# Performance work log

Measured on AMD Instinct MI355X. Metric: run time of the kernel, lower is better.

The kernel has to match this reference:

```python
import jax, jax.numpy as jnp
import numpy as np

B, T, M, D, H, DK, DV = 2, 1024, 1024, 1024, 16, 64, 64
R = 2 * T + M  # number of relative positions required by rel_shift path


def setup_inputs() -> dict:
    key = jax.random.key(0)
    ks = jax.random.split(key, 11)
    s = 0.02
    return {
        "inputs": jax.random.normal(ks[0], (B, T, D), jnp.float32),
        "attention_mask": jnp.ones((B, T, M + T), jnp.float32),
        "positional_encodings": jax.random.normal(ks[1], (R, D), jnp.float32),
        "memory": jax.random.normal(ks[2], (B, M, D), jnp.float32),
        "Wq": jax.random.normal(ks[3], (D, H * DK), jnp.float32) * s,
        "Wk": jax.random.normal(ks[4], (D, H * DK), jnp.float32) * s,
        "Wv": jax.random.normal(ks[5], (D, H * DV), jnp.float32) * s,
        "Wr": jax.random.normal(ks[6], (D, H * DK), jnp.float32) * s,
        "r_w_bias": jax.random.normal(ks[7], (H, DK), jnp.float32) * s,
        "r_r_bias": jax.random.normal(ks[8], (H, DK), jnp.float32) * s,
        "W_out": jax.random.normal(ks[9], (H * DV, D), jnp.float32) * s,
    }


def _rel_shift(m, attention_length):
    # m: [T_q, T_q + L] -> [T_q, L], TXL relative shift via reshape/slice
    tq, total = m.shape
    x = m.reshape(total, tq)[1:].reshape(tq, total - 1)
    return x[:, :attention_length]


def reference(inputs, attention_mask, positional_encodings, memory,
              Wq, Wk, Wv, Wr, r_w_bias, r_r_bias, W_out):
    b, t, d = inputs.shape
    values = jnp.concatenate([memory, inputs], axis=1)  # [B, L, D]
    L = values.shape[1]
    q = (inputs @ Wq).reshape(b, t, H, DK)
    k = (values @ Wk).reshape(b, L, H, DK)
    v = (values @ Wv).reshape(b, L, H, DV)
    rk = (positional_encodings @ Wr).reshape(-1, H, DK)  # [R, H, DK]
    # content + relative logits (TXL)
    content = jnp.einsum('bthd,bThd->bhtT', q + r_w_bias, k)        # [B,H,T,L]
    rel = jnp.einsum('bthd,rhd->bhtr', q + r_r_bias, rk)            # [B,H,T,R]
    rel = jax.vmap(jax.vmap(lambda m: _rel_shift(m, L)))(rel)       # [B,H,T,L]
    logits = (content + rel) * (DK ** -0.5)
    masked = logits - (1.0 - attention_mask[:, None, :, :]) * 1e30
    w = jax.nn.softmax(masked, axis=-1)
    attn = jnp.einsum('bhtT,bThd->bthd', w, v)                      # [B,T,H,DV]
    return attn.reshape(b, t, H * DV) @ W_out
```

## Files before the change

### kernel.cpp

```cpp
#include <hip/hip_runtime.h>
#include <hip/hip_fp16.h>
#include <stdint.h>

#define Bz 2
#define Tq 1024
#define Mm 1024
#define Hh 16
#define Ll 2048
#define Rr 3072

typedef __attribute__((ext_vector_type(8))) short bf16x8;
typedef __attribute__((ext_vector_type(4))) float f32x4;

typedef __attribute__((address_space(3))) uint8_t lds_u8_t;
typedef __attribute__((address_space(1))) uint8_t glb_u8_t;

__device__ __forceinline__ void gl2lds16(const void* g, void* l) {
  __builtin_amdgcn_global_load_lds((const glb_u8_t*)g, (lds_u8_t*)l, 16, 0, 0);
}

__device__ __forceinline__ unsigned short f2bf(float f) {
  unsigned int u = __builtin_bit_cast(unsigned int, f);
  u = u + 0x7fffu + ((u >> 16) & 1u);
  return (unsigned short)(u >> 16);
}
__device__ __forceinline__ float b2f(unsigned short s) {
  unsigned int u = ((unsigned int)s) << 16;
  return __builtin_bit_cast(float, u);
}

__global__ __launch_bounds__(256) void k_prep2(
    const float* __restrict__ x, const float* __restrict__ mem,
    const float* __restrict__ pos, const float* __restrict__ mask,
    const float* __restrict__ w0, const float* __restrict__ w1,
    const float* __restrict__ w2, const float* __restrict__ w3,
    const float* __restrict__ w4,
    unsigned short* __restrict__ vin, unsigned short* __restrict__ pb,
    unsigned short* __restrict__ mb,
    unsigned short* __restrict__ t0, unsigned short* __restrict__ t1,
    unsigned short* __restrict__ t2, unsigned short* __restrict__ t3,
    unsigned short* __restrict__ t4) {
  __shared__ float tile[64][65];
  int bid = blockIdx.x;
  if (bid < 4096) {
    int idx = bid * 256 + threadIdx.x;
    int e = idx << 2;
    int row = e >> 10, col = e & 1023;
    int b = row >> 11, l = row & 2047;
    const float* s = (l < Mm) ? (mem + (((size_t)b * Mm + l) << 10) + col)
                              : (x + (((size_t)b * Tq + (l - Mm)) << 10) + col);
    float4 v = *(const float4*)s;
    ushort4 o;
    o.x = f2bf(v.x); o.y = f2bf(v.y); o.z = f2bf(v.z); o.w = f2bf(v.w);
    *(ushort4*)(vin + e) = o;
  } else if (bid < 7168) {
    int idx = (bid - 4096) * 256 + threadIdx.x;
    int e = idx << 2;
    float4 v = *(const float4*)(pos + e);
    ushort4 t;
    t.x = f2bf(v.x); t.y = f2bf(v.y); t.z = f2bf(v.z); t.w = f2bf(v.w);
    *(ushort4*)(pb + e) = t;
  } else if (bid < 11264) {
    int idx = (bid - 7168) * 256 + threadIdx.x;
    int e = idx << 2;
    const float BIGM = 1.442695e30f;
    float4 v = *(const float4*)(mask + e);
    ushort4 t;
    t.x = f2bf((1.0f - v.x) * BIGM); t.y = f2bf((1.0f - v.y) * BIGM);
    t.z = f2bf((1.0f - v.z) * BIGM); t.w = f2bf((1.0f - v.w) * BIGM);
    *(ushort4*)(mb + e) = t;
  } else {
    int r3 = bid - 11264;
    int mz = r3 >> 8, rem = r3 & 255;
    const float* W;
    unsigned short* WT;
    switch (mz) {
      case 0: W = w0; WT = t0; break;
      case 1: W = w1; WT = t1; break;
      case 2: W = w2; WT = t2; break;
      case 3: W = w3; WT = t3; break;
      default: W = w4; WT = t4; break;
    }
    int k0 = (rem >> 4) * 64, n0 = (rem & 15) * 64;
    int tid = threadIdx.x;
    int rr = tid >> 4, c4 = (tid & 15) * 4;
#pragma unroll
    for (int it = 0; it < 4; ++it) {
      int r = rr + it * 16;
      float4 v = *(const float4*)(W + (size_t)(k0 + r) * 1024 + n0 + c4);
      tile[r][c4] = v.x; tile[r][c4 + 1] = v.y;
      tile[r][c4 + 2] = v.z; tile[r][c4 + 3] = v.w;
    }
    __syncthreads();
#pragma unroll
    for (int it = 0; it < 4; ++it) {
      int n = rr + it * 16;
      ushort4 o;
      o.x = f2bf(tile[c4 + 0][n]); o.y = f2bf(tile[c4 + 1][n]);
      o.z = f2bf(tile[c4 + 2][n]); o.w = f2bf(tile[c4 + 3][n]);
      *(ushort4*)(WT + (size_t)(n0 + n) * 1024 + k0 + c4) = o;
    }
  }
}

template <int RMAP>
__device__ __forceinline__ void gemm_pipe(const unsigned short* __restrict__ A,
                                          const unsigned short* __restrict__ Bt,
                                          int m0, int n0, unsigned short* As,
                                          unsigned short* Bs, f32x4 acc[4][4]) {
  const int tid = threadIdx.x;
  const int w = tid >> 6, lane = tid & 63;
  const int quad = lane >> 4, li = lane & 15;
  const int wr = w >> 1, wc = w & 1;
  f32x4 z = {0.f, 0.f, 0.f, 0.f};
#pragma unroll
  for (int mi = 0; mi < 4; ++mi)
#pragma unroll
    for (int ni = 0; ni < 4; ++ni) acc[mi][ni] = z;

  const int rs = lane >> 2;
  const int cs = lane & 3;

#pragma unroll
  for (int s = 0; s < 2; ++s) {
    int i = w * 2 + s;
    int r = i * 16 + rs;
    int c = cs ^ ((r >> 1) & 3);
    int ar = m0 + r;
    if (RMAP) ar = ar + 1024 + (ar & 1024);
    gl2lds16(A + (size_t)ar * 1024 + c * 8, (char*)As + i * 1024);
    gl2lds16(Bt + (size_t)(n0 + r) * 1024 + c * 8, (char*)Bs + i * 1024);
  }

  for (int k0 = 0; k0 < 1024; k0 += 32) {
    const int bo = ((k0 >> 5) & 1) * 8192;
    const int no = bo ^ 8192;
    __builtin_amdgcn_s_waitcnt(0x0F70);
    __syncthreads();
    if (k0 + 32 < 1024) {
#pragma unroll
      for (int s = 0; s < 2; ++s) {
        int i = w * 2 + s;
        int r = i * 16 + rs;
        int c = cs ^ ((r >> 1) & 3);
        int ar = m0 + r;
        if (RMAP) ar = ar + 1024 + (ar & 1024);
        gl2lds16(A + (size_t)ar * 1024 + k0 + 32 + c * 8,
                 (char*)As + no + i * 1024);
        gl2lds16(Bt + (size_t)(n0 + r) * 1024 + k0 + 32 + c * 8,
                 (char*)Bs + no + i * 1024);
      }
    }
    bf16x8 af[4], bfr[4];
#pragma unroll
    for (int mi = 0; mi < 4; ++mi) {
      int r = wr * 64 + mi * 16 + li;
      int ch = quad ^ ((r >> 1) & 3);
      af[mi] = *(const bf16x8*)((const char*)As + bo + r * 64 + ch * 16);
    }
#pragma unroll
    for (int ni = 0; ni < 4; ++ni) {
      int r = wc * 64 + ni * 16 + li;
      int ch = quad ^ ((r >> 1) & 3);
      bfr[ni] = *(const bf16x8*)((const char*)Bs + bo + r * 64 + ch * 16);
    }
#pragma unroll
    for (int mi = 0; mi < 4; ++mi)
#pragma unroll
      for (int ni = 0; ni < 4; ++ni)
        acc[mi][ni] = __builtin_amdgcn_mfma_f32_16x16x32_bf16(
            af[mi], bfr[ni], acc[mi][ni], 0, 0, 0);
  }
}

__global__ __launch_bounds__(256) void k_proj(
    const unsigned short* __restrict__ Vin, const unsigned short* __restrict__ Pb,
    const unsigned short* __restrict__ WqT, const unsigned short* __restrict__ WkT,
    const unsigned short* __restrict__ WvT, const unsigned short* __restrict__ WrT,
    unsigned short* __restrict__ qb, unsigned short* __restrict__ kb,
    unsigned short* __restrict__ vtb, unsigned short* __restrict__ rkb) {
  __shared__ unsigned short As[2 * 128 * 32];
  __shared__ unsigned short Bs[2 * 128 * 32];
  const int t = blockIdx.x;
  const int tid = threadIdx.x, w = tid >> 6, lane = tid & 63;
  const int quad = lane >> 4, li = lane & 15, wr = w >> 1, wc = w & 1;
  f32x4 acc[4][4];

  if (t < 256) {
    int m0 = (t >> 3) * 128, n0 = (t & 7) * 128;
    gemm_pipe<0>(Vin, WkT, m0, n0, As, Bs, acc);
#pragma unroll
    for (int mi = 0; mi < 4; ++mi)
#pragma unroll
      for (int ni = 0; ni < 4; ++ni)
#pragma unroll
        for (int reg = 0; reg < 4; ++reg) {
          int rrow = m0 + wr * 64 + mi * 16 + quad * 4 + reg;
          int cc = n0 + wc * 64 + ni * 16 + li;
          kb[(size_t)rrow * 1024 + cc] = f2bf(acc[mi][ni][reg]);
        }
  } else if (t < 512) {
    int tt = t - 256;
    int m0 = (tt >> 3) * 128, n0 = (tt & 7) * 128;
    gemm_pipe<0>(Vin, WvT, m0, n0, As, Bs, acc);
#pragma unroll
    for (int mi = 0; mi < 4; ++mi)
#pragma unroll
      for (int ni = 0; ni < 4; ++ni) {
        int r0 = m0 + wr * 64 + mi * 16 + quad * 4;
        int b = r0 >> 11, l0 = r0 & 2047;
        int cc = n0 + wc * 64 + ni * 16 + li;
        ushort4 o;
        o.x = f2bf(acc[mi][ni][0]); o.y = f2bf(acc[mi][ni][1]);
        o.z = f2bf(acc[mi][ni][2]); o.w = f2bf(acc[mi][ni][3]);
        *(ushort4*)(vtb + ((size_t)(b * 1024 + cc)) * Ll + l0) = o;
      }
  } else if (t < 640) {
    int tt = t - 512;
    int m0 = (tt >> 3) * 128, n0 = (tt & 7) * 128;
    gemm_pipe<1>(Vin, WqT, m0, n0, As, Bs, acc);
#pragma unroll
    for (int mi = 0; mi < 4; ++mi)
#pragma unroll
      for (int ni = 0; ni < 4; ++ni)
#pragma unroll
        for (int reg = 0; reg < 4; ++reg) {
          int rrow = m0 + wr * 64 + mi * 16 + quad * 4 + reg;
          int cc = n0 + wc * 64 + ni * 16 + li;
          qb[(size_t)rrow * 1024 + cc] = f2bf(acc[mi][ni][reg]);
        }
  } else {
    int tt = t - 640;
    int m0 = (tt >> 3) * 128, n0 = (tt & 7) * 128;
    gemm_pipe<0>(Pb, WrT, m0, n0, As, Bs, acc);
#pragma unroll
    for (int mi = 0; mi < 4; ++mi)
#pragma unroll
      for (int ni = 0; ni < 4; ++ni)
#pragma unroll
        for (int reg = 0; reg < 4; ++reg) {
          int rrow = m0 + wr * 64 + mi * 16 + quad * 4 + reg;
          int cc = n0 + wc * 64 + ni * 16 + li;
          rkb[(size_t)rrow * 1024 + cc] = f2bf(acc[mi][ni][reg]);
        }
  }
}

__global__ __launch_bounds__(256) void k_gemm_out64(
    const unsigned short* __restrict__ attnb, const unsigned short* __restrict__ WoT,
    float* __restrict__ out) {
  __shared__ unsigned short As[2 * 64 * 32];
  __shared__ unsigned short Bs[2 * 128 * 32];
  int m0 = blockIdx.x * 64, n0 = blockIdx.y * 128;
  const int tid = threadIdx.x, w = tid >> 6, lane = tid & 63;
  const int quad = lane >> 4, li = lane & 15, wr = w >> 1, wc = w & 1;
  f32x4 z = {0.f, 0.f, 0.f, 0.f};
  f32x4 acc[2][4];
#pragma unroll
  for (int mi = 0; mi < 2; ++mi)
#pragma unroll
    for (int ni = 0; ni < 4; ++ni) acc[mi][ni] = z;
  const int rs = lane >> 2, cs = lane & 3;

  {
    int r = w * 16 + rs;
    int c = cs ^ ((r >> 1) & 3);
    gl2lds16(attnb + (size_t)(m0 + r) * 1024 + c * 8, (char*)As + w * 1024);
  }
#pragma unroll
  for (int s = 0; s < 2; ++s) {
    int i = w * 2 + s;
    int r = i * 16 + rs;
    int c = cs ^ ((r >> 1) & 3);
    gl2lds16(WoT + (size_t)(n0 + r) * 1024 + c * 8, (char*)Bs + i * 1024);
  }

  for (int k0 = 0; k0 < 1024; k0 += 32) {
    const int boa = ((k0 >> 5) & 1) * 4096;
    const int bob = ((k0 >> 5) & 1) * 8192;
    __builtin_amdgcn_s_waitcnt(0x0F70);
    __syncthreads();
    if (k0 + 32 < 1024) {
      {
        int r = w * 16 + rs;
        int c = cs ^ ((r >> 1) & 3);
        gl2lds16(attnb + (size_t)(m0 + r) * 1024 + k0 + 32 + c * 8,
                 (char*)As + (boa ^ 4096) + w * 1024);
      }
#pragma unroll
      for (int s = 0; s < 2; ++s) {
        int i = w * 2 + s;
        int r = i * 16 + rs;
        int c = cs ^ ((r >> 1) & 3);
        gl2lds16(WoT + (size_t)(n0 + r) * 1024 + k0 + 32 + c * 8,
                 (char*)Bs + (bob ^ 8192) + i * 1024);
      }
    }
    bf16x8 af[2], bfr[4];
#pragma unroll
    for (int mi = 0; mi < 2; ++mi) {
      int r = wr * 32 + mi * 16 + li;
      int ch = quad ^ ((r >> 1) & 3);
      af[mi] = *(const bf16x8*)((const char*)As + boa + r * 64 + ch * 16);
    }
#pragma unroll
    for (int ni = 0; ni < 4; ++ni) {
      int r = wc * 64 + ni * 16 + li;
      int ch = quad ^ ((r >> 1) & 3);
      bfr[ni] = *(const bf16x8*)((const char*)Bs + bob + r * 64 + ch * 16);
    }
#pragma unroll
    for (int mi = 0; mi < 2; ++mi)
#pragma unroll
      for (int ni = 0; ni < 4; ++ni)
        acc[mi][ni] = __builtin_amdgcn_mfma_f32_16x16x32_bf16(
            af[mi], bfr[ni], acc[mi][ni], 0, 0, 0);
  }
#pragma unroll
  for (int mi = 0; mi < 2; ++mi)
#pragma unroll
    for (int ni = 0; ni < 4; ++ni)
#pragma unroll
      for (int reg = 0; reg < 4; ++reg) {
        int rrow = m0 + wr * 32 + mi * 16 + quad * 4 + reg;
        int cc = n0 + wc * 64 + ni * 16 + li;
        out[(size_t)rrow * 1024 + cc] = acc[mi][ni][reg];
      }
}

__global__ __launch_bounds__(256, 2) void k_attn(
    const unsigned short* __restrict__ qb, const float* __restrict__ rwb,
    const float* __restrict__ rrb,
    const unsigned short* __restrict__ kb, const unsigned short* __restrict__ vt,
    const unsigned short* __restrict__ rkb, const unsigned short* __restrict__ mb,
    unsigned short* __restrict__ attnb) {
  __shared__ unsigned short Ks[2][64 * 64];
  __shared__ unsigned short Vs[2][64 * 64];
  __shared__ unsigned short Rs[256 * 64];
  __shared__ unsigned short Sb[4][16 * 72];

  const int tid = threadIdx.x;
  const int w = tid >> 6, lane = tid & 63;
  const int quad = lane >> 4, li = lane & 15;
  const int flat = blockIdx.x + 16 * blockIdx.y + 256 * blockIdx.z;
  const int qt = (flat >> 3) & 15;
  const int g = 4 * (flat & 7) + (flat >> 7);
  const int h = g & 15, b = g >> 4;
  const int t0blk = qt * 64;
  const int t0w = t0blk + w * 16;
  const int rboff = 48 - 16 * w;
  const int rbase0 = Tq - t0blk - 63;

  bf16x8 aqw[2], aqr[2];
  {
    const unsigned short* p1 = qb + ((size_t)((b * Tq + t0w + li) * Hh + h)) * 64;
#pragma unroll
    for (int ks = 0; ks < 2; ++ks) {
      bf16x8 qf = *(const bf16x8*)(p1 + ks * 32 + quad * 8);
      const float* wp = rwb + h * 64 + ks * 32 + quad * 8;
      const float* rp = rrb + h * 64 + ks * 32 + quad * 8;
      float4 w0 = *(const float4*)wp, w1 = *(const float4*)(wp + 4);
      float4 r0 = *(const float4*)rp, r1 = *(const float4*)(rp + 4);
      float wv[8] = {w0.x, w0.y, w0.z, w0.w, w1.x, w1.y, w1.z, w1.w};
      float rv[8] = {r0.x, r0.y, r0.z, r0.w, r1.x, r1.y, r1.z, r1.w};
#pragma unroll
      for (int i2 = 0; i2 < 8; ++i2) {
        float qv = b2f((unsigned short)qf[i2]);
        aqw[ks][i2] = (short)f2bf(qv + wv[i2]);
        aqr[ks][i2] = (short)f2bf(qv + rv[i2]);
      }
    }
  }

  f32x4 z = {0.f, 0.f, 0.f, 0.f};
  f32x4 o[4];
  o[0] = z; o[1] = z; o[2] = z; o[3] = z;
  f32x4 ol = z;

  const int srow = lane >> 3;
  const int scs = lane & 7;
  const float SC = 0.125f * 1.4426950408889634f;
  const short oneb = 0x3F80;
  const bf16x8 onesf = {oneb, oneb, oneb, oneb, oneb, oneb, oneb, oneb};

  unsigned short* pw = &Sb[w][0];
  const unsigned short* mrowA = mb + ((size_t)(b * Tq + t0w + li)) * Ll;
  int srcl[4];
#pragma unroll
  for (int reg = 0; reg < 4; ++reg) {
    int row = quad * 4 + reg;
    srcl[reg] = (lane & 48) + ((li + row + 1) & 15);
  }

  auto finish = [&](const unsigned short* VsP, bf16x8 mvF0, bf16x8 mvF1) {
    bf16x8 apv[2];
#pragma unroll
    for (int ks = 0; ks < 2; ++ks) {
      const int cofs = ks * 32 + quad * 8;
      ushort4 s0 = *(const ushort4*)(pw + li * 72 + cofs);
      ushort4 s1 = *(const ushort4*)(pw + li * 72 + cofs + 4);
      bf16x8 mv = ks ? mvF1 : mvF0;
      unsigned short su[8] = {s0.x, s0.y, s0.z, s0.w, s1.x, s1.y, s1.z, s1.w};
#pragma unroll
      for (int i2 = 0; i2 < 8; ++i2) {
        float sf = __half2float(__builtin_bit_cast(__half, su[i2]));
        float mvf = b2f((unsigned short)mv[i2]);
        float p = exp2f(sf * SC - mvf);
        apv[ks][i2] = (short)f2bf(p);
      }
    }
    __builtin_amdgcn_s_setprio(1);
#pragma unroll
    for (int ks = 0; ks < 2; ++ks)
      ol = __builtin_amdgcn_mfma_f32_16x16x32_bf16(apv[ks], onesf, ol, 0, 0, 0);
#pragma unroll
    for (int ks = 0; ks < 2; ++ks)
#pragma unroll
      for (int nt = 0; nt < 4; ++nt) {
        int dv = nt * 16 + li;
        int ch = (ks * 4 + quad) ^ (dv & 7);
        bf16x8 vf = *(const bf16x8*)((const char*)VsP + dv * 128 + ch * 16);
        o[nt] = __builtin_amdgcn_mfma_f32_16x16x32_bf16(apv[ks], vf, o[nt], 0, 0, 0);
      }
    __builtin_amdgcn_s_setprio(0);
  };

#pragma unroll
  for (int s = 0; s < 4; ++s) {
    int i = w * 4 + s;
    int r = i * 8 + srow;
    int gr = rbase0 + r;
    if (gr > Rr - 1) gr = Rr - 1;
    int c = scs ^ (r & 7);
    gl2lds16(rkb + ((size_t)gr * Hh + h) * 64 + c * 8, (char*)Rs + i * 1024);
  }
#pragma unroll
  for (int s = 0; s < 2; ++s) {
    int i = w * 2 + s;
    int r = i * 8 + srow;
    int c = scs ^ (r & 7);
    gl2lds16(kb + ((size_t)((b * Ll + r) * Hh + h)) * 64 + c * 8,
             (char*)Ks[0] + i * 1024);
  }
  bf16x8 nmv0 = {0, 0, 0, 0, 0, 0, 0, 0};
  bf16x8 nmv1 = {0, 0, 0, 0, 0, 0, 0, 0};

  for (int jt = 0; jt < 32; ++jt) {
    const int j0 = jt * 64;
    __builtin_amdgcn_s_waitcnt(0x0F70);
    __syncthreads();
    bf16x8 mvF0 = nmv0, mvF1 = nmv1;
    if (jt < 31) {
      const int j0n = j0 + 64;
#pragma unroll
      for (int s = 0; s < 2; ++s) {
        int i = w * 2 + s;
        int r = i * 8 + srow;
        int c = scs ^ (r & 7);
        gl2lds16(kb + ((size_t)((b * Ll + j0n + r) * Hh + h)) * 64 + c * 8,
                 (char*)Ks[(jt + 1) & 1] + i * 1024);
      }
#pragma unroll
      for (int s = 0; s < 2; ++s) {
        int i2 = w * 2 + s;
        int rr = i2 * 8 + srow;
        int ofs = j0 + 128 + rr;
        int gr = rbase0 + ofs;
        if (gr > Rr - 1) gr = Rr - 1;
        int ring = ofs & 255;
        int c = scs ^ (rr & 7);
        gl2lds16(rkb + ((size_t)gr * Hh + h) * 64 + c * 8, (char*)Rs + ring * 128);
      }
    }
#pragma unroll
    for (int s = 0; s < 2; ++s) {
      int i = w * 2 + s;
      int r = i * 8 + srow;
      int c = scs ^ (r & 7);
      gl2lds16(vt + ((size_t)((b * Hh + h) * 64 + r)) * Ll + j0 + c * 8,
               (char*)Vs[jt & 1] + i * 1024);
    }
    nmv0 = *(const bf16x8*)(mrowA + j0 + quad * 8);
    nmv1 = *(const bf16x8*)(mrowA + j0 + 32 + quad * 8);
    asm volatile("" ::: "memory");
    const unsigned short* KsC = Ks[jt & 1];
    f32x4 sc[4];
    sc[0] = z; sc[1] = z; sc[2] = z; sc[3] = z;
    __builtin_amdgcn_s_setprio(1);
#pragma unroll
    for (int ks = 0; ks < 2; ++ks)
#pragma unroll
      for (int nt = 0; nt < 4; ++nt) {
        int j = nt * 16 + li;
        int ch = (ks * 4 + quad) ^ (j & 7);
        bf16x8 kf = *(const bf16x8*)((const char*)KsC + j * 128 + ch * 16);
        sc[nt] = __builtin_amdgcn_mfma_f32_16x16x32_bf16(aqw[ks], kf, sc[nt], 0, 0, 0);
      }
    f32x4 bd[5];
    bd[0] = z; bd[1] = z; bd[2] = z; bd[3] = z; bd[4] = z;
#pragma unroll
    for (int ks = 0; ks < 2; ++ks)
#pragma unroll
      for (int nt = 0; nt < 5; ++nt) {
        int pr = (rboff + nt * 16 + li + j0) & 255;
        int ch = (ks * 4 + quad) ^ (pr & 7);
        bf16x8 rf = *(const bf16x8*)((const char*)Rs + pr * 128 + ch * 16);
        bd[nt] = __builtin_amdgcn_mfma_f32_16x16x32_bf16(aqr[ks], rf, bd[nt], 0, 0, 0);
      }
    __builtin_amdgcn_s_setprio(0);
    if (jt > 0) finish(Vs[(jt - 1) & 1], mvF0, mvF1);
    float rot[4][4];
#pragma unroll
    for (int nt = 0; nt < 4; ++nt)
#pragma unroll
      for (int reg = 0; reg < 4; ++reg)
        rot[nt][reg] = __shfl(sc[nt][reg], srcl[reg], 64);
#pragma unroll
    for (int nt = 0; nt < 5; ++nt)
#pragma unroll
      for (int reg = 0; reg < 4; ++reg) {
        int row = quad * 4 + reg;
        int jj = nt * 16 + li + row - 15;
        int ntlo = (nt == 0) ? 3 : (nt - 1);
        int nthi = (nt > 3) ? 0 : nt;
        float val = ((li + row) >= 15) ? rot[nthi][reg] : rot[ntlo][reg];
        float s = val + bd[nt][reg];
        if ((unsigned)jj < 64u)
          pw[row * 72 + jj] = __builtin_bit_cast(unsigned short, __float2half(s));
      }
  }
  __builtin_amdgcn_s_waitcnt(0x0F70);
  __syncthreads();
  finish(Vs[1], nmv0, nmv1);

  float inv[4];
#pragma unroll
  for (int reg = 0; reg < 4; ++reg) inv[reg] = 1.0f / ol[reg];
#pragma unroll
  for (int nt = 0; nt < 4; ++nt)
#pragma unroll
    for (int reg = 0; reg < 4; ++reg) {
      int trow = t0w + quad * 4 + reg;
      attnb[((size_t)(b * Tq + trow)) * 1024 + h * 64 + nt * 16 + li] =
          f2bf(o[nt][reg] * inv[reg]);
    }
}

extern "C" void kernel_launch(void* const* d_in, const int* in_sizes, int n_in,
                              void* d_out, int out_size, void* d_ws, size_t ws_size,
                              hipStream_t stream) {
  const float* x = (const float*)d_in[0];
  const float* mask = (const float*)d_in[1];
  const float* pos = (const float*)d_in[2];
  const float* mem = (const float*)d_in[3];
  const float* Wq = (const float*)d_in[4];
  const float* Wk = (const float*)d_in[5];
  const float* Wv = (const float*)d_in[6];
  const float* Wr = (const float*)d_in[7];
  const float* rwb = (const float*)d_in[8];
  const float* rrb = (const float*)d_in[9];
  const float* Wo = (const float*)d_in[10];
  float* out = (float*)d_out;

  uint8_t* ws = (uint8_t*)d_ws;
  const size_t MB = 1024 * 1024;
  unsigned short* Vinb = (unsigned short*)(ws + 0);
  unsigned short* WqT = (unsigned short*)(ws + 8 * MB);
  unsigned short* WkT = (unsigned short*)(ws + 10 * MB);
  unsigned short* WvT = (unsigned short*)(ws + 12 * MB);
  unsigned short* WrT = (unsigned short*)(ws + 14 * MB);
  unsigned short* WoT = (unsigned short*)(ws + 16 * MB);
  unsigned short* Pb = (unsigned short*)(ws + 18 * MB);
  unsigned short* qb = (unsigned short*)(ws + 24 * MB);
  unsigned short* kb = (unsigned short*)(ws + 32 * MB);
  unsigned short* vtb = (unsigned short*)(ws + 40 * MB);
  unsigned short* rkb = (unsigned short*)(ws + 48 * MB);
  unsigned short* mbb = (unsigned short*)(ws + 54 * MB);
  unsigned short* attnb = (unsigned short*)(ws + 19 * MB);

  hipLaunchKernelGGL(k_prep2, dim3(12544), dim3(256), 0, stream,
                     x, mem, pos, mask, Wq, Wk, Wv, Wr, Wo,
                     Vinb, Pb, mbb, WqT, WkT, WvT, WrT, WoT);
  hipLaunchKernelGGL(k_proj, dim3(832), dim3(256), 0, stream,
                     Vinb, Pb, WqT, WkT, WvT, WrT, qb, kb, vtb, rkb);
  hipLaunchKernelGGL(k_attn, dim3(16, 16, 2), dim3(256), 0, stream,
                     qb, rwb, rrb, kb, vtb, rkb, mbb, attnb);
  hipLaunchKernelGGL(k_gemm_out64, dim3(32, 8), dim3(256), 0, stream,
                     attnb, WoT, out);
}
```

Baseline: 253.2 us.

## Split attention key range across two wave groups with LDS reduction

The attention kernel now launches 512 threads per block, where two groups of four waves each process half of the key/value length (1024 positions) in 32-wide tiles instead of 64-wide tiles. Each group keeps its own K, V and relative-position LDS buffers. At the end, the partial output and row-sum accumulators are combined through LDS before normalisation. The aim is more waves in flight to hide latency within the same grid, at the cost of an extra reduction, a larger LDS footprint (about 74KB) and smaller MFMA tiles per iteration.

```diff
diff --git a/kernel.cpp b/kernel.cpp
--- a/kernel.cpp
+++ b/kernel.cpp
@@ -328,28 +328,39 @@
       }
 }
 
-__global__ __launch_bounds__(256, 2) void k_attn(
+__global__ __launch_bounds__(512, 4) void k_attn(
     const unsigned short* __restrict__ qb, const float* __restrict__ rwb,
     const float* __restrict__ rrb,
     const unsigned short* __restrict__ kb, const unsigned short* __restrict__ vt,
     const unsigned short* __restrict__ rkb, const unsigned short* __restrict__ mb,
     unsigned short* __restrict__ attnb) {
-  __shared__ unsigned short Ks[2][64 * 64];
-  __shared__ unsigned short Vs[2][64 * 64];
-  __shared__ unsigned short Rs[256 * 64];
-  __shared__ unsigned short Sb[4][16 * 72];
+  __shared__ __align__(16) uint8_t lds[75776];
 
   const int tid = threadIdx.x;
   const int w = tid >> 6, lane = tid & 63;
   const int quad = lane >> 4, li = lane & 15;
+  const int wq = w & 3, grp = w >> 2;
+  const int srow = lane >> 3, scs = lane & 7;
   const int flat = blockIdx.x + 16 * blockIdx.y + 256 * blockIdx.z;
   const int qt = (flat >> 3) & 15;
   const int g = 4 * (flat & 7) + (flat >> 7);
   const int h = g & 15, b = g >> 4;
   const int t0blk = qt * 64;
-  const int t0w = t0blk + w * 16;
-  const int rboff = 48 - 16 * w;
+  const int t0w = t0blk + wq * 16;
+  const int rboff = 48 - 16 * wq;
   const int rbase0 = Tq - t0blk - 63;
+  const int jbase = grp * 1024;
+
+  unsigned short* KS = (unsigned short*)(lds + grp * 8192);
+  unsigned short* VS = (unsigned short*)(lds + 16384 + grp * 8192);
+  unsigned short* RS = (unsigned short*)(lds + 32768 + grp * 16384);
+  unsigned short* pw = (unsigned short*)(lds + 65536 + w * 1280);
+  float* red = (float*)(lds + 32768);
+
+  const unsigned short* kbase = kb + ((size_t)(b * Ll + jbase) * Hh + h) * 64;
+  const unsigned short* vbase = vt + ((size_t)((b * Hh + h) * 64)) * Ll + jbase;
+  const unsigned short* rkbase = rkb + (size_t)h * 64;
+  const unsigned short* mrow = mb + ((size_t)(b * Tq + t0w + li)) * Ll + jbase;
 
   bf16x8 aqw[2], aqr[2];
   {
@@ -376,15 +387,12 @@
   f32x4 o[4];
   o[0] = z; o[1] = z; o[2] = z; o[3] = z;
   f32x4 ol = z;
-
-  const int srow = lane >> 3;
-  const int scs = lane & 7;
+  bf16x8 nmv = {0, 0, 0, 0, 0, 0, 0, 0};
+
   const float SC = 0.125f * 1.4426950408889634f;
   const short oneb = 0x3F80;
   const bf16x8 onesf = {oneb, oneb, oneb, oneb, oneb, oneb, oneb, oneb};
 
-  unsigned short* pw = &Sb[w][0];
-  const unsigned short* mrowA = mb + ((size_t)(b * Tq + t0w + li)) * Ll;
   int srcl[4];
 #pragma unroll
   for (int reg = 0; reg < 4; ++reg) {
@@ -392,158 +400,144 @@
     srcl[reg] = (lane & 48) + ((li + row + 1) & 15);
   }
 
-  auto finish = [&](const unsigned short* VsP, bf16x8 mvF0, bf16x8 mvF1) {
-    bf16x8 apv[2];
-#pragma unroll
-    for (int ks = 0; ks < 2; ++ks) {
-      const int cofs = ks * 32 + quad * 8;
-      ushort4 s0 = *(const ushort4*)(pw + li * 72 + cofs);
-      ushort4 s1 = *(const ushort4*)(pw + li * 72 + cofs + 4);
-      bf16x8 mv = ks ? mvF1 : mvF0;
-      unsigned short su[8] = {s0.x, s0.y, s0.z, s0.w, s1.x, s1.y, s1.z, s1.w};
-#pragma unroll
-      for (int i2 = 0; i2 < 8; ++i2) {
-        float sf = __half2float(__builtin_bit_cast(__half, su[i2]));
-        float mvf = b2f((unsigned short)mv[i2]);
-        float p = exp2f(sf * SC - mvf);
-        apv[ks][i2] = (short)f2bf(p);
-      }
+  auto finish = [&](const unsigned short* VsP, bf16x8 mv) {
+    bf16x8 sv = *(const bf16x8*)(pw + li * 40 + quad * 8);
+    bf16x8 apv;
+#pragma unroll
+    for (int i2 = 0; i2 < 8; ++i2) {
+      float sf = __half2float(__builtin_bit_cast(__half, (unsigned short)sv[i2]));
+      float mvf = b2f((unsigned short)mv[i2]);
+      float p = exp2f(sf * SC - mvf);
+      apv[i2] = (short)f2bf(p);
     }
     __builtin_amdgcn_s_setprio(1);
-#pragma unroll
-    for (int ks = 0; ks < 2; ++ks)
-      ol = __builtin_amdgcn_mfma_f32_16x16x32_bf16(apv[ks], onesf, ol, 0, 0, 0);
-#pragma unroll
-    for (int ks = 0; ks < 2; ++ks)
-#pragma unroll
-      for (int nt = 0; nt < 4; ++nt) {
-        int dv = nt * 16 + li;
-        int ch = (ks * 4 + quad) ^ (dv & 7);
-        bf16x8 vf = *(const bf16x8*)((const char*)VsP + dv * 128 + ch * 16);
-        o[nt] = __builtin_amdgcn_mfma_f32_16x16x32_bf16(apv[ks], vf, o[nt], 0, 0, 0);
-      }
+    ol = __builtin_amdgcn_mfma_f32_16x16x32_bf16(apv, onesf, ol, 0, 0, 0);
+#pragma unroll
+    for (int nt = 0; nt < 4; ++nt) {
+      int dv = nt * 16 + li;
+      int ch = quad ^ (dv & 3);
+      bf16x8 vf = *(const bf16x8*)(VsP + dv * 32 + ch * 8);
+      o[nt] = __builtin_amdgcn_mfma_f32_16x16x32_bf16(apv, vf, o[nt], 0, 0, 0);
+    }
     __builtin_amdgcn_s_setprio(0);
   };
 
 #pragma unroll
-  for (int s = 0; s < 4; ++s) {
-    int i = w * 4 + s;
-    int r = i * 8 + srow;
-    int gr = rbase0 + r;
+  for (int pass = 0; pass < 3; ++pass) {
+    int u = pass * 32 + wq * 8 + srow;
+    int gr = rbase0 + jbase + u;
     if (gr > Rr - 1) gr = Rr - 1;
-    int c = scs ^ (r & 7);
-    gl2lds16(rkb + ((size_t)gr * Hh + h) * 64 + c * 8, (char*)Rs + i * 1024);
-  }
-#pragma unroll
-  for (int s = 0; s < 2; ++s) {
-    int i = w * 2 + s;
-    int r = i * 8 + srow;
-    int c = scs ^ (r & 7);
-    gl2lds16(kb + ((size_t)((b * Ll + r) * Hh + h)) * 64 + c * 8,
-             (char*)Ks[0] + i * 1024);
-  }
-  bf16x8 nmv0 = {0, 0, 0, 0, 0, 0, 0, 0};
-  bf16x8 nmv1 = {0, 0, 0, 0, 0, 0, 0, 0};
+    int c = scs ^ srow;
+    gl2lds16(rkbase + (size_t)gr * 1024 + c * 8, RS + (pass * 32 + wq * 8) * 64);
+  }
+  {
+    int r = wq * 8 + srow;
+    int c = scs ^ srow;
+    gl2lds16(kbase + (size_t)r * 1024 + c * 8, KS + wq * 512);
+  }
 
   for (int jt = 0; jt < 32; ++jt) {
-    const int j0 = jt * 64;
+    const int jloc = jt * 32;
     __builtin_amdgcn_s_waitcnt(0x0F70);
     __syncthreads();
-    bf16x8 mvF0 = nmv0, mvF1 = nmv1;
     if (jt < 31) {
-      const int j0n = j0 + 64;
-#pragma unroll
-      for (int s = 0; s < 2; ++s) {
-        int i = w * 2 + s;
-        int r = i * 8 + srow;
-        int c = scs ^ (r & 7);
-        gl2lds16(kb + ((size_t)((b * Ll + j0n + r) * Hh + h)) * 64 + c * 8,
-                 (char*)Ks[(jt + 1) & 1] + i * 1024);
-      }
-#pragma unroll
-      for (int s = 0; s < 2; ++s) {
-        int i2 = w * 2 + s;
-        int rr = i2 * 8 + srow;
-        int ofs = j0 + 128 + rr;
-        int gr = rbase0 + ofs;
+      {
+        int r = wq * 8 + srow;
+        int c = scs ^ srow;
+        gl2lds16(kbase + (size_t)(jloc + 32 + r) * 1024 + c * 8,
+                 KS + (((jt + 1) & 1) * 2048) + wq * 512);
+      }
+      {
+        int u = jloc + 96 + wq * 8 + srow;
+        int gr = rbase0 + jbase + u;
         if (gr > Rr - 1) gr = Rr - 1;
-        int ring = ofs & 255;
-        int c = scs ^ (rr & 7);
-        gl2lds16(rkb + ((size_t)gr * Hh + h) * 64 + c * 8, (char*)Rs + ring * 128);
-      }
-    }
-#pragma unroll
-    for (int s = 0; s < 2; ++s) {
-      int i = w * 2 + s;
-      int r = i * 8 + srow;
-      int c = scs ^ (r & 7);
-      gl2lds16(vt + ((size_t)((b * Hh + h) * 64 + r)) * Ll + j0 + c * 8,
-               (char*)Vs[jt & 1] + i * 1024);
-    }
-    nmv0 = *(const bf16x8*)(mrowA + j0 + quad * 8);
-    nmv1 = *(const bf16x8*)(mrowA + j0 + 32 + quad * 8);
+        int c = scs ^ srow;
+        gl2lds16(rkbase + (size_t)gr * 1024 + c * 8,
+                 RS + ((jloc + 96 + wq * 8) & 127) * 64);
+      }
+    }
+    {
+      int dv = wq * 16 + (lane >> 2);
+      int c = (lane & 3) ^ (dv & 3);
+      gl2lds16(vbase + (size_t)dv * Ll + jloc + c * 8,
+               VS + ((jt & 1) * 2048) + wq * 512);
+    }
     asm volatile("" ::: "memory");
-    const unsigned short* KsC = Ks[jt & 1];
-    f32x4 sc[4];
-    sc[0] = z; sc[1] = z; sc[2] = z; sc[3] = z;
+    const unsigned short* KsC = KS + (jt & 1) * 2048;
+    f32x4 sc[2];
+    sc[0] = z; sc[1] = z;
     __builtin_amdgcn_s_setprio(1);
 #pragma unroll
     for (int ks = 0; ks < 2; ++ks)
 #pragma unroll
-      for (int nt = 0; nt < 4; ++nt) {
+      for (int nt = 0; nt < 2; ++nt) {
         int j = nt * 16 + li;
         int ch = (ks * 4 + quad) ^ (j & 7);
-        bf16x8 kf = *(const bf16x8*)((const char*)KsC + j * 128 + ch * 16);
+        bf16x8 kf = *(const bf16x8*)(KsC + j * 64 + ch * 8);
         sc[nt] = __builtin_amdgcn_mfma_f32_16x16x32_bf16(aqw[ks], kf, sc[nt], 0, 0, 0);
       }
-    f32x4 bd[5];
-    bd[0] = z; bd[1] = z; bd[2] = z; bd[3] = z; bd[4] = z;
+    f32x4 bd[3];
+    bd[0] = z; bd[1] = z; bd[2] = z;
 #pragma unroll
     for (int ks = 0; ks < 2; ++ks)
 #pragma unroll
-      for (int nt = 0; nt < 5; ++nt) {
-        int pr = (rboff + nt * 16 + li + j0) & 255;
+      for (int nt = 0; nt < 3; ++nt) {
+        int pr = (rboff + nt * 16 + li + jloc) & 127;
         int ch = (ks * 4 + quad) ^ (pr & 7);
-        bf16x8 rf = *(const bf16x8*)((const char*)Rs + pr * 128 + ch * 16);
+        bf16x8 rf = *(const bf16x8*)(RS + pr * 64 + ch * 8);
         bd[nt] = __builtin_amdgcn_mfma_f32_16x16x32_bf16(aqr[ks], rf, bd[nt], 0, 0, 0);
       }
     __builtin_amdgcn_s_setprio(0);
-    if (jt > 0) finish(Vs[(jt - 1) & 1], mvF0, mvF1);
-    float rot[4][4];
-#pragma unroll
-    for (int nt = 0; nt < 4; ++nt)
+    if (jt > 0) finish(VS + ((jt - 1) & 1) * 2048, nmv);
+    nmv = *(const bf16x8*)(mrow + jloc + quad * 8);
+    float rot[2][4];
+#pragma unroll
+    for (int nt = 0; nt < 2; ++nt)
 #pragma unroll
       for (int reg = 0; reg < 4; ++reg)
         rot[nt][reg] = __shfl(sc[nt][reg], srcl[reg], 64);
 #pragma unroll
-    for (int nt = 0; nt < 5; ++nt)
+    for (int nt = 0; nt < 3; ++nt)
 #pragma unroll
       for (int reg = 0; reg < 4; ++reg) {
         int row = quad * 4 + reg;
         int jj = nt * 16 + li + row - 15;
-        int ntlo = (nt == 0) ? 3 : (nt - 1);
-        int nthi = (nt > 3) ? 0 : nt;
+        int nthi = (nt > 1) ? 0 : nt;
+        int ntlo = (nt == 0) ? 0 : (nt - 1);
         float val = ((li + row) >= 15) ? rot[nthi][reg] : rot[ntlo][reg];
         float s = val + bd[nt][reg];
-        if ((unsigned)jj < 64u)
-          pw[row * 72 + jj] = __builtin_bit_cast(unsigned short, __float2half(s));
+        if ((unsigned)jj < 32u)
+          pw[row * 40 + jj] = __builtin_bit_cast(unsigned short, __float2half(s));
       }
   }
   __builtin_amdgcn_s_waitcnt(0x0F70);
   __syncthreads();
-  finish(Vs[1], nmv0, nmv1);
-
-  float inv[4];
-#pragma unroll
-  for (int reg = 0; reg < 4; ++reg) inv[reg] = 1.0f / ol[reg];
-#pragma unroll
-  for (int nt = 0; nt < 4; ++nt)
-#pragma unroll
-    for (int reg = 0; reg < 4; ++reg) {
-      int trow = t0w + quad * 4 + reg;
-      attnb[((size_t)(b * Tq + trow)) * 1024 + h * 64 + nt * 16 + li] =
-          f2bf(o[nt][reg] * inv[reg]);
-    }
+  finish(VS + 2048, nmv);
+
+  if (grp == 1) {
+    float* rp = red + (size_t)(wq * 64 + lane) * 20;
+#pragma unroll
+    for (int nt = 0; nt < 4; ++nt)
+#pragma unroll
+      for (int reg = 0; reg < 4; ++reg) rp[nt * 4 + reg] = o[nt][reg];
+#pragma unroll
+    for (int reg = 0; reg < 4; ++reg) rp[16 + reg] = ol[reg];
+  }
+  __syncthreads();
+  if (grp == 0) {
+    const float* rp = red + (size_t)(wq * 64 + lane) * 20;
+    float inv[4];
+#pragma unroll
+    for (int reg = 0; reg < 4; ++reg) inv[reg] = 1.0f / (ol[reg] + rp[16 + reg]);
+#pragma unroll
+    for (int nt = 0; nt < 4; ++nt)
+#pragma unroll
+      for (int reg = 0; reg < 4; ++reg) {
+        int trow = t0w + quad * 4 + reg;
+        float val = (o[nt][reg] + rp[nt * 4 + reg]) * inv[reg];
+        attnb[((size_t)(b * Tq + trow)) * 1024 + h * 64 + nt * 16 + li] = f2bf(val);
+      }
+  }
 }
 
 extern "C" void kernel_launch(void* const* d_in, const int* in_sizes, int n_in,
@@ -583,7 +577,7 @@
                      Vinb, Pb, mbb, WqT, WkT, WvT, WrT, WoT);
   hipLaunchKernelGGL(k_proj, dim3(832), dim3(256), 0, stream,
                      Vinb, Pb, WqT, WkT, WvT, WrT, qb, kb, vtb, rkb);
-  hipLaunchKernelGGL(k_attn, dim3(16, 16, 2), dim3(256), 0, stream,
+  hipLaunchKernelGGL(k_attn, dim3(16, 16, 2), dim3(512), 0, stream,
                      qb, rwb, rrb, kb, vtb, rkb, mbb, attnb);
   hipLaunchKernelGGL(k_gemm_out64, dim3(32, 8), dim3(256), 0, stream,
                      attnb, WoT, out);
```

After: 252.7 us. No clear change (-0.2%).
